# Kernel tuning notes

Measured on AMD Instinct MI355X. Metric: run time of the kernel, lower is better.

## Reference

```python
import jax, jax.numpy as jnp
import numpy as np

FORWARD_BITS = 8
R_MAX = 0.01
SIGMA0_FWD = 2.0 ** (6 - FORWARD_BITS)  # 0.25, per DynamicFixedQuantizer.__init__


def _rescale(data, sigma, bit, r_max):
    """Dynamic range adjustment: doubles sigma on overflow, halves on underflow."""
    half = 2.0 ** (bit - 1)
    t_max = sigma * half - sigma
    t_min = -sigma * half
    n = jnp.float32(data.size)
    overflow = (jnp.sum(data > t_max) + jnp.sum(data < t_min)).astype(jnp.float32) / n
    underflow = (jnp.sum(data > 0.5 * t_max) + jnp.sum(data < 0.5 * t_min)).astype(jnp.float32) / n
    sigma = jnp.where(overflow > r_max, sigma * 2.0,
                      jnp.where(underflow < r_max, sigma * 0.5, sigma))
    t_max = sigma * half - sigma
    t_min = -sigma * half
    return sigma, t_min, t_max


def _stochastic_round(data, sigma, t_min, t_max, key):
    # temp = floor(data/sigma + U[0,1)) * sigma, then clamp -- fused elementwise chain
    r = jax.random.uniform(key, data.shape, dtype=data.dtype)
    temp = jnp.floor(data / sigma + r) * sigma
    return jnp.clip(temp, t_min, t_max)


def setup_inputs() -> dict:
    key = jax.random.key(0)
    x = jax.random.normal(key, (32, 2048, 2048), dtype=jnp.float32)
    return {"x": x}


def reference(x):
    sigma = jnp.float32(SIGMA0_FWD)
    sigma, t_min, t_max = _rescale(x, sigma, FORWARD_BITS, R_MAX)
    # forward always uses stochastic rounding in the original code
    rkey = jax.random.fold_in(jax.random.key(42), 0)
    return _stochastic_round(x, sigma, t_min, t_max, rkey)
```

## Files before the change

kernel.cpp:

```cpp
#include <hip/hip_runtime.h>
#include <stdint.h>

static inline void threefry2x32_host(uint32_t k0, uint32_t k1,
                                     uint32_t x0, uint32_t x1,
                                     uint32_t& o0, uint32_t& o1) {
  const uint32_t ks2 = k0 ^ k1 ^ 0x1BD11BDAu;
#define TF_ROUND(r) { x0 += x1; x1 = (x1 << (r)) | (x1 >> (32 - (r))); x1 ^= x0; }
  x0 += k0; x1 += k1;
  TF_ROUND(13) TF_ROUND(15) TF_ROUND(26) TF_ROUND(6)
  x0 += k1;  x1 += ks2 + 1u;
  TF_ROUND(17) TF_ROUND(29) TF_ROUND(16) TF_ROUND(24)
  x0 += ks2; x1 += k0 + 2u;
  TF_ROUND(13) TF_ROUND(15) TF_ROUND(26) TF_ROUND(6)
  x0 += k0;  x1 += k1 + 3u;
  TF_ROUND(17) TF_ROUND(29) TF_ROUND(16) TF_ROUND(24)
  x0 += k1;  x1 += ks2 + 4u;
  TF_ROUND(13) TF_ROUND(15) TF_ROUND(26) TF_ROUND(6)
  x0 += ks2; x1 += k0 + 5u;
#undef TF_ROUND
  o0 = x0; o1 = x1;
}

__device__ __forceinline__ uint32_t tf_bits(uint32_t x1, uint32_t k0,
                                            uint32_t k1, uint32_t ks2) {
  uint32_t x0 = k0;
#define R4(a,b,c,d)                                              \
  x0 += x1; x1 = __builtin_rotateleft32(x1, a); x1 ^= x0;        \
  x0 += x1; x1 = __builtin_rotateleft32(x1, b); x1 ^= x0;        \
  x0 += x1; x1 = __builtin_rotateleft32(x1, c); x1 ^= x0;        \
  x0 += x1; x1 = __builtin_rotateleft32(x1, d); x1 ^= x0;
  R4(13, 15, 26, 6)
  x0 += k1;  x1 += ks2 + 1u;
  R4(17, 29, 16, 24)
  x0 += ks2; x1 += k0 + 2u;
  R4(13, 15, 26, 6)
  x0 += k0;  x1 += k1 + 3u;
  R4(17, 29, 16, 24)
  x0 += k1;  x1 += ks2 + 4u;
  R4(13, 15, 26, 6)
  x0 += ks2; x1 += k0 + 5u;
#undef R4
  return x0 ^ x1;
}

__device__ __forceinline__ float qround(float v, uint32_t bits, float sigma,
                                        float inv_sigma, float tmin, float tmax) {
  float r = __uint_as_float((bits >> 9) | 0x3f800000u) - 1.0f;
  float t = floorf(__builtin_fmaf(v, inv_sigma, r)) * sigma;
  return fminf(fmaxf(t, tmin), tmax);
}

__global__ __launch_bounds__(256) void count_kernel(
    const float4* __restrict__ x4, const float* __restrict__ x,
    long long n4, long long n, unsigned int* __restrict__ counts,
    float tmax, float tmin, float htmax, float htmin) {
  long long i = (long long)blockIdx.x * 256 + threadIdx.x;
  unsigned int over = 0, under = 0;
  if (i < n4) {
    float4 v = x4[i];
    over  = __popcll(__ballot(v.x > tmax))  + __popcll(__ballot(v.x < tmin))
          + __popcll(__ballot(v.y > tmax))  + __popcll(__ballot(v.y < tmin))
          + __popcll(__ballot(v.z > tmax))  + __popcll(__ballot(v.z < tmin))
          + __popcll(__ballot(v.w > tmax))  + __popcll(__ballot(v.w < tmin));
    under = __popcll(__ballot(v.x > htmax)) + __popcll(__ballot(v.x < htmin))
          + __popcll(__ballot(v.y > htmax)) + __popcll(__ballot(v.y < htmin))
          + __popcll(__ballot(v.z > htmax)) + __popcll(__ballot(v.z < htmin))
          + __popcll(__ballot(v.w > htmax)) + __popcll(__ballot(v.w < htmin));
  }
  if ((threadIdx.x & 63) == 0) {
    if (over)  atomicAdd(&counts[0], over);
    if (under) atomicAdd(&counts[1], under);
  }
  if (i == 0 && (n & 3)) {
    unsigned int o2 = 0, u2 = 0;
    for (long long j = n4 << 2; j < n; ++j) {
      float v = x[j];
      o2 += (v > tmax)  + (v < tmin);
      u2 += (v > htmax) + (v < htmin);
    }
    if (o2) atomicAdd(&counts[0], o2);
    if (u2) atomicAdd(&counts[1], u2);
  }
}

__global__ __launch_bounds__(256) void quant_kernel(
    const float4* __restrict__ x4, float4* __restrict__ o4,
    const float* __restrict__ x, float* __restrict__ out,
    long long n4, long long n, const unsigned int* __restrict__ counts,
    float inv_n, uint32_t k0, uint32_t k1) {
  const uint32_t ks2 = k0 ^ k1 ^ 0x1BD11BDAu;
  float overflow  = (float)counts[0] * inv_n;
  float underflow = (float)counts[1] * inv_n;
  float sigma = (overflow > 0.01f) ? 0.5f
              : ((underflow < 0.01f) ? 0.125f : 0.25f);
  float tmax = sigma * 128.0f - sigma;
  float tmin = sigma * -128.0f;
  float inv_sigma = 1.0f / sigma;

  long long i = (long long)blockIdx.x * 256 + threadIdx.x;
  if (i < n4) {
    float4 v = x4[i];
    uint32_t s = ((uint32_t)i << 2) + k1;
    uint32_t b0 = tf_bits(s + 0u, k0, k1, ks2);
    uint32_t b1 = tf_bits(s + 1u, k0, k1, ks2);
    uint32_t b2 = tf_bits(s + 2u, k0, k1, ks2);
    uint32_t b3 = tf_bits(s + 3u, k0, k1, ks2);
    v.x = qround(v.x, b0, sigma, inv_sigma, tmin, tmax);
    v.y = qround(v.y, b1, sigma, inv_sigma, tmin, tmax);
    v.z = qround(v.z, b2, sigma, inv_sigma, tmin, tmax);
    v.w = qround(v.w, b3, sigma, inv_sigma, tmin, tmax);
    o4[i] = v;
  }
  if (i == 0 && (n & 3)) {
    for (long long j = n4 << 2; j < n; ++j) {
      uint32_t b = tf_bits((uint32_t)j + k1, k0, k1, ks2);
      out[j] = qround(x[j], b, sigma, inv_sigma, tmin, tmax);
    }
  }
}

extern "C" void kernel_launch(void* const* d_in, const int* in_sizes, int n_in,
                              void* d_out, int out_size, void* d_ws, size_t ws_size,
                              hipStream_t stream) {
  const float* x = (const float*)d_in[0];
  float* out = (float*)d_out;
  long long n = (long long)in_sizes[0];

  unsigned int* counts = (unsigned int*)d_ws;
  hipMemsetAsync(counts, 0, 2 * sizeof(unsigned int), stream);

  uint32_t k0, k1;
  threefry2x32_host(0u, 42u, 0u, 0u, k0, k1);

  const float sigma0 = 0.25f;
  const float tmax0 = sigma0 * 128.0f - sigma0;
  const float tmin0 = -sigma0 * 128.0f;
  const float htmax0 = 0.5f * tmax0;
  const float htmin0 = 0.5f * tmin0;

  long long n4 = n >> 2;
  long long grid = (n4 + 255) / 256;
  if (grid < 1) grid = 1;

  count_kernel<<<(dim3)(unsigned)grid, 256, 0, stream>>>(
      (const float4*)x, x, n4, n, counts, tmax0, tmin0, htmax0, htmin0);

  float inv_n = 1.0f / (float)n;
  quant_kernel<<<(dim3)(unsigned)grid, 256, 0, stream>>>(
      (const float4*)x, (float4*)out, x, out, n4, n, counts, inv_n, k0, k1);
}
```

Baseline: 1.004 ms.

## Use grid-stride loops, reverse quant traversal for cache reuse, nontemporal stores

```diff
diff --git a/kernel.cpp b/kernel.cpp
--- a/kernel.cpp
+++ b/kernel.cpp
@@ -1,5 +1,7 @@
 #include <hip/hip_runtime.h>
 #include <stdint.h>
+
+typedef float floatx4 __attribute__((ext_vector_type(4)));
 
 static inline void threefry2x32_host(uint32_t k0, uint32_t k1,
                                      uint32_t x0, uint32_t x1,
@@ -54,24 +56,25 @@
     const float4* __restrict__ x4, const float* __restrict__ x,
     long long n4, long long n, unsigned int* __restrict__ counts,
     float tmax, float tmin, float htmax, float htmin) {
-  long long i = (long long)blockIdx.x * 256 + threadIdx.x;
+  long long idx = (long long)blockIdx.x * 256 + threadIdx.x;
+  long long stride = (long long)gridDim.x * 256;
   unsigned int over = 0, under = 0;
-  if (i < n4) {
+  for (long long i = idx; i < n4; i += stride) {
     float4 v = x4[i];
-    over  = __popcll(__ballot(v.x > tmax))  + __popcll(__ballot(v.x < tmin))
-          + __popcll(__ballot(v.y > tmax))  + __popcll(__ballot(v.y < tmin))
-          + __popcll(__ballot(v.z > tmax))  + __popcll(__ballot(v.z < tmin))
-          + __popcll(__ballot(v.w > tmax))  + __popcll(__ballot(v.w < tmin));
-    under = __popcll(__ballot(v.x > htmax)) + __popcll(__ballot(v.x < htmin))
-          + __popcll(__ballot(v.y > htmax)) + __popcll(__ballot(v.y < htmin))
-          + __popcll(__ballot(v.z > htmax)) + __popcll(__ballot(v.z < htmin))
-          + __popcll(__ballot(v.w > htmax)) + __popcll(__ballot(v.w < htmin));
+    over  += __popcll(__ballot(v.x > tmax))  + __popcll(__ballot(v.x < tmin))
+           + __popcll(__ballot(v.y > tmax))  + __popcll(__ballot(v.y < tmin))
+           + __popcll(__ballot(v.z > tmax))  + __popcll(__ballot(v.z < tmin))
+           + __popcll(__ballot(v.w > tmax))  + __popcll(__ballot(v.w < tmin));
+    under += __popcll(__ballot(v.x > htmax)) + __popcll(__ballot(v.x < htmin))
+           + __popcll(__ballot(v.y > htmax)) + __popcll(__ballot(v.y < htmin))
+           + __popcll(__ballot(v.z > htmax)) + __popcll(__ballot(v.z < htmin))
+           + __popcll(__ballot(v.w > htmax)) + __popcll(__ballot(v.w < htmin));
   }
   if ((threadIdx.x & 63) == 0) {
     if (over)  atomicAdd(&counts[0], over);
     if (under) atomicAdd(&counts[1], under);
   }
-  if (i == 0 && (n & 3)) {
+  if (idx == 0 && (n & 3)) {
     unsigned int o2 = 0, u2 = 0;
     for (long long j = n4 << 2; j < n; ++j) {
       float v = x[j];
@@ -84,7 +87,7 @@
 }
 
 __global__ __launch_bounds__(256) void quant_kernel(
-    const float4* __restrict__ x4, float4* __restrict__ o4,
+    const float4* __restrict__ x4, floatx4* __restrict__ o4,
     const float* __restrict__ x, float* __restrict__ out,
     long long n4, long long n, const unsigned int* __restrict__ counts,
     float inv_n, uint32_t k0, uint32_t k1) {
@@ -97,21 +100,26 @@
   float tmin = sigma * -128.0f;
   float inv_sigma = 1.0f / sigma;
 
-  long long i = (long long)blockIdx.x * 256 + threadIdx.x;
-  if (i < n4) {
-    float4 v = x4[i];
-    uint32_t s = ((uint32_t)i << 2) + k1;
-    uint32_t b0 = tf_bits(s + 0u, k0, k1, ks2);
-    uint32_t b1 = tf_bits(s + 1u, k0, k1, ks2);
-    uint32_t b2 = tf_bits(s + 2u, k0, k1, ks2);
-    uint32_t b3 = tf_bits(s + 3u, k0, k1, ks2);
-    v.x = qround(v.x, b0, sigma, inv_sigma, tmin, tmax);
-    v.y = qround(v.y, b1, sigma, inv_sigma, tmin, tmax);
-    v.z = qround(v.z, b2, sigma, inv_sigma, tmin, tmax);
-    v.w = qround(v.w, b3, sigma, inv_sigma, tmin, tmax);
-    o4[i] = v;
+  long long idx = (long long)blockIdx.x * 256 + threadIdx.x;
+  long long stride = (long long)gridDim.x * 256;
+  if (idx < n4) {
+    long long i = idx + ((n4 - 1 - idx) / stride) * stride;
+    for (; i >= idx; i -= stride) {
+      float4 v = x4[i];
+      uint32_t s = ((uint32_t)i << 2) + k1;
+      uint32_t b0 = tf_bits(s + 0u, k0, k1, ks2);
+      uint32_t b1 = tf_bits(s + 1u, k0, k1, ks2);
+      uint32_t b2 = tf_bits(s + 2u, k0, k1, ks2);
+      uint32_t b3 = tf_bits(s + 3u, k0, k1, ks2);
+      floatx4 r;
+      r.x = qround(v.x, b0, sigma, inv_sigma, tmin, tmax);
+      r.y = qround(v.y, b1, sigma, inv_sigma, tmin, tmax);
+      r.z = qround(v.z, b2, sigma, inv_sigma, tmin, tmax);
+      r.w = qround(v.w, b3, sigma, inv_sigma, tmin, tmax);
+      __builtin_nontemporal_store(r, &o4[i]);
+    }
   }
-  if (i == 0 && (n & 3)) {
+  if (idx == 0 && (n & 3)) {
     for (long long j = n4 << 2; j < n; ++j) {
       uint32_t b = tf_bits((uint32_t)j + k1, k0, k1, ks2);
       out[j] = qround(x[j], b, sigma, inv_sigma, tmin, tmax);
@@ -127,7 +135,7 @@
   long long n = (long long)in_sizes[0];
 
   unsigned int* counts = (unsigned int*)d_ws;
-  hipMemsetAsync(counts, 0, 2 * sizeof(unsigned int), stream);
+  (void)hipMemsetAsync(counts, 0, 2 * sizeof(unsigned int), stream);
 
   uint32_t k0, k1;
   threefry2x32_host(0u, 42u, 0u, 0u, k0, k1);
@@ -141,11 +149,12 @@
   long long n4 = n >> 2;
   long long grid = (n4 + 255) / 256;
   if (grid < 1) grid = 1;
+  if (grid > 2048) grid = 2048;
 
   count_kernel<<<(dim3)(unsigned)grid, 256, 0, stream>>>(
       (const float4*)x, x, n4, n, counts, tmax0, tmin0, htmax0, htmin0);
 
   float inv_n = 1.0f / (float)n;
   quant_kernel<<<(dim3)(unsigned)grid, 256, 0, stream>>>(
-      (const float4*)x, (float4*)out, x, out, n4, n, counts, inv_n, k0, k1);
+      (const float4*)x, (floatx4*)out, x, out, n4, n, counts, inv_n, k0, k1);
 }
```

Result: slower. 1.075 ms (+7.1%).
